# Optimization experiments

Measured on AMD Instinct MI355X. Metric: run time of the kernel, lower is better.

## Reference

```python
import jax, jax.numpy as jnp
import numpy as np

B, T, D_IN, D_ENC, D_H = 16384, 60, 3, 64, 128


def setup_inputs() -> dict:
    key = jax.random.key(0)
    ks = jax.random.split(key, 10)
    s_enc = 1.0 / np.sqrt(D_IN)
    s_lstm = 1.0 / np.sqrt(D_H)
    s_dec = 1.0 / np.sqrt(D_H)
    return {
        "x": jax.random.normal(ks[0], (B, D_IN), dtype=jnp.float32),
        "W_enc": jax.random.uniform(ks[1], (D_ENC, D_IN), jnp.float32, -s_enc, s_enc),
        "b_enc": jax.random.uniform(ks[2], (D_ENC,), jnp.float32, -s_enc, s_enc),
        "W_ih": jax.random.uniform(ks[3], (4 * D_H, D_ENC), jnp.float32, -s_lstm, s_lstm),
        "W_hh": jax.random.uniform(ks[4], (4 * D_H, D_H), jnp.float32, -s_lstm, s_lstm),
        "b_ih": jax.random.uniform(ks[5], (4 * D_H,), jnp.float32, -s_lstm, s_lstm),
        "b_hh": jax.random.uniform(ks[6], (4 * D_H,), jnp.float32, -s_lstm, s_lstm),
        "W_dec": jax.random.uniform(ks[7], (1, D_H), jnp.float32, -s_dec, s_dec),
        "b_dec": jax.random.uniform(ks[8], (1,), jnp.float32, -s_dec, s_dec),
    }


def _forward(x, W_enc, b_enc, W_ih, W_hh, b_ih, b_hh, W_dec, b_dec):
    encoded = x @ W_enc.T + b_enc  # [B, 64]
    # Input to LSTM is identical at every timestep -> precompute Wx projection once.
    xp = encoded @ W_ih.T + b_ih + b_hh  # [B, 4*H], PyTorch gate order i,f,g,o
    h0 = jnp.zeros((x.shape[0], D_H), x.dtype)
    c0 = jnp.zeros((x.shape[0], D_H), x.dtype)

    def step(carry, _):
        h, c = carry
        gates = xp + h @ W_hh.T  # [B, 4*H]
        i, f, g, o = jnp.split(gates, 4, axis=-1)
        i = jax.nn.sigmoid(i)
        f = jax.nn.sigmoid(f)
        g = jnp.tanh(g)
        o = jax.nn.sigmoid(o)
        c = f * c + i * g
        h = o * jnp.tanh(c)
        return (h, c), h

    (_, _), hs = jax.lax.scan(step, (h0, c0), None, length=T)  # hs: [T, B, H]
    lstm_out = jnp.transpose(hs, (1, 0, 2))  # [B, T, H]
    out = (lstm_out @ W_dec.T + b_dec)[..., 0]  # [B, T]
    return jax.nn.sigmoid(out)


def reference(x, W_enc, b_enc, W_ih, W_hh, b_ih, b_hh, W_dec, b_dec):
    return _forward(x, W_enc, b_enc, W_ih, W_hh, b_ih, b_hh, W_dec, b_dec)
```

## Files before the change

### kernel.cpp

```cpp
#include <hip/hip_runtime.h>

#define T_STEPS 60
#define HID 128
#define ROWS 16
#define NBLK (16384 / ROWS)

typedef __attribute__((ext_vector_type(8))) short short8;
typedef __attribute__((ext_vector_type(4))) float f32x4;

#define K1 1.44269504088896340736f

__device__ __forceinline__ unsigned short f2bf(float f) {
  unsigned u = __float_as_uint(f);
  return (unsigned short)((u + 0x7fffu + ((u >> 16) & 1u)) >> 16);
}
__device__ __forceinline__ float sigm(float x) {
  return __builtin_amdgcn_rcpf(1.0f + __expf(-x));
}
template <int CTRL>
__device__ __forceinline__ float dppadd(float x) {
  int y = __builtin_amdgcn_update_dpp(0, __builtin_bit_cast(int, x), CTRL, 0xf,
                                      0xf, false);
  return x + __builtin_bit_cast(float, y);
}

#define HB0 0
#define HB1 4096
#define XP_BASE 8192
#define PART 40960
#define WSTRIDE 968
#define LDS_BYTES (PART + 8 * WSTRIDE * 4)

__global__ __launch_bounds__(512, 4) void lstm_fused(
    const float* __restrict__ x, const float* __restrict__ W_enc,
    const float* __restrict__ b_enc, const float* __restrict__ W_ih,
    const float* __restrict__ W_hh, const float* __restrict__ b_ih,
    const float* __restrict__ b_hh, const float* __restrict__ W_dec,
    const float* __restrict__ b_dec, float* __restrict__ out) {
  __shared__ __align__(16) unsigned char lds[LDS_BYTES];

  const int tid = threadIdx.x;
  const int wav = tid >> 6;
  const int lane = tid & 63;
  const int l15 = lane & 15;
  const int l4 = lane >> 4;
  const int u = wav * 16 + l15;
  const int row0 = blockIdx.x * ROWS;

  for (int i = tid; i < 1024; i += 512) ((unsigned*)(lds + HB0))[i] = 0u;

  {
    f32x4 xp4[4];
    float xr0[4], xr1[4], xr2[4];
#pragma unroll
    for (int v = 0; v < 4; ++v) {
      int r = 4 * l4 + v;
      const float* xp_ = x + (size_t)(row0 + r) * 3;
      xr0[v] = xp_[0];
      xr1[v] = xp_[1];
      xr2[v] = xp_[2];
    }
#pragma unroll
    for (int gt = 0; gt < 4; ++gt) {
      float bias = b_ih[gt * 128 + u] + b_hh[gt * 128 + u];
#pragma unroll
      for (int v = 0; v < 4; ++v) xp4[gt][v] = bias;
    }
    const f32x4* wr0 = (const f32x4*)(W_ih + (size_t)u * 64);
    const f32x4* wr1 = (const f32x4*)(W_ih + (size_t)(128 + u) * 64);
    const f32x4* wr2 = (const f32x4*)(W_ih + (size_t)(256 + u) * 64);
    const f32x4* wr3 = (const f32x4*)(W_ih + (size_t)(384 + u) * 64);
    for (int e4 = 0; e4 < 16; ++e4) {
      f32x4 w0 = wr0[e4], w1 = wr1[e4], w2 = wr2[e4], w3 = wr3[e4];
#pragma unroll
      for (int j = 0; j < 4; ++j) {
        int e = e4 * 4 + j;
        float we0 = W_enc[e * 3], we1 = W_enc[e * 3 + 1], we2 = W_enc[e * 3 + 2];
        float be = b_enc[e];
#pragma unroll
        for (int v = 0; v < 4; ++v) {
          float ev = fmaf(we0, xr0[v], fmaf(we1, xr1[v], fmaf(we2, xr2[v], be)));
          xp4[0][v] = fmaf(w0[j], ev, xp4[0][v]);
          xp4[1][v] = fmaf(w1[j], ev, xp4[1][v]);
          xp4[2][v] = fmaf(w2[j], ev, xp4[2][v]);
          xp4[3][v] = fmaf(w3[j], ev, xp4[3][v]);
        }
      }
    }
#pragma unroll
    for (int gt = 0; gt < 4; ++gt) {
      float s = (gt == 2) ? (-2.0f * K1) : (-K1);
#pragma unroll
      for (int v = 0; v < 4; ++v) xp4[gt][v] *= s;
      *(f32x4*)(lds + XP_BASE + gt * 8192 + (unsigned)tid * 16) = xp4[gt];
    }
  }

  short8 bw[4][4];
#pragma unroll
  for (int gt = 0; gt < 4; ++gt) {
    float s = (gt == 2) ? (-2.0f * K1) : (-K1);
#pragma unroll
    for (int kt = 0; kt < 4; ++kt) {
      const float* p = W_hh + (size_t)(gt * 128 + u) * HID + kt * 32 + 8 * l4;
      short8 f;
#pragma unroll
      for (int j = 0; j < 8; ++j) f[j] = (short)f2bf(s * p[j]);
      bw[gt][kt] = f;
    }
  }

  float ct0 = 0.0f, ct1 = 0.0f, ct2 = 0.0f, ct3 = 0.0f;

  const unsigned swzA =
      (((unsigned)(l15 & 7)) << 4) ^ (((unsigned)(l15 & 8)) << 2);
  unsigned rd0 = ((unsigned)(l15 * 256 + l4 * 16)) ^ swzA;
  unsigned rd1 = ((unsigned)(l15 * 256 + l4 * 16 + 64)) ^ swzA;
  unsigned wr0, wr1, wr2, wr3;
  {
    unsigned rr = (unsigned)(4 * l4);
#define WRADDR(v) ((((rr + v) * 256 + (unsigned)u * 2) ^ (((rr + v) & 7u) << 4) ^ \
                    (((rr + v) & 8u) << 2)) + HB1)
    wr0 = WRADDR(0); wr1 = WRADDR(1); wr2 = WRADDR(2); wr3 = WRADDR(3);
#undef WRADDR
  }
  const unsigned xpA = (unsigned)tid * 16;
  const float wdu = W_dec[u];
  unsigned ptv = PART + (unsigned)(wav * WSTRIDE + 4 * l4) * 4;
  const float kneg = -2.0f * K1;
  const float kpos = 2.0f * K1;

  __syncthreads();

#pragma clang loop unroll(disable)
  for (int t = 0; t < T_STEPS; ++t) {
    f32x4 xpr0 = *(const f32x4*)(lds + XP_BASE + 0 * 8192 + xpA);
    f32x4 xpr1 = *(const f32x4*)(lds + XP_BASE + 1 * 8192 + xpA);
    f32x4 xpr2 = *(const f32x4*)(lds + XP_BASE + 2 * 8192 + xpA);
    f32x4 xpr3 = *(const f32x4*)(lds + XP_BASE + 3 * 8192 + xpA);
    short8 af0 = *(const short8*)(lds + rd0);
    short8 af1 = *(const short8*)(lds + rd1);
    short8 af2 = *(const short8*)(lds + rd0 + 128);
    short8 af3 = *(const short8*)(lds + rd1 + 128);
    f32x4 a0 = __builtin_amdgcn_mfma_f32_16x16x32_bf16(af0, bw[0][0], xpr0, 0, 0, 0);
    f32x4 a1 = __builtin_amdgcn_mfma_f32_16x16x32_bf16(af0, bw[1][0], xpr1, 0, 0, 0);
    f32x4 a2 = __builtin_amdgcn_mfma_f32_16x16x32_bf16(af0, bw[2][0], xpr2, 0, 0, 0);
    f32x4 a3 = __builtin_amdgcn_mfma_f32_16x16x32_bf16(af0, bw[3][0], xpr3, 0, 0, 0);
    a0 = __builtin_amdgcn_mfma_f32_16x16x32_bf16(af1, bw[0][1], a0, 0, 0, 0);
    a1 = __builtin_amdgcn_mfma_f32_16x16x32_bf16(af1, bw[1][1], a1, 0, 0, 0);
    a2 = __builtin_amdgcn_mfma_f32_16x16x32_bf16(af1, bw[2][1], a2, 0, 0, 0);
    a3 = __builtin_amdgcn_mfma_f32_16x16x32_bf16(af1, bw[3][1], a3, 0, 0, 0);
    a0 = __builtin_amdgcn_mfma_f32_16x16x32_bf16(af2, bw[0][2], a0, 0, 0, 0);
    a1 = __builtin_amdgcn_mfma_f32_16x16x32_bf16(af2, bw[1][2], a1, 0, 0, 0);
    a2 = __builtin_amdgcn_mfma_f32_16x16x32_bf16(af2, bw[2][2], a2, 0, 0, 0);
    a3 = __builtin_amdgcn_mfma_f32_16x16x32_bf16(af2, bw[3][2], a3, 0, 0, 0);
    a0 = __builtin_amdgcn_mfma_f32_16x16x32_bf16(af3, bw[0][3], a0, 0, 0, 0);
    a1 = __builtin_amdgcn_mfma_f32_16x16x32_bf16(af3, bw[1][3], a1, 0, 0, 0);
    a2 = __builtin_amdgcn_mfma_f32_16x16x32_bf16(af3, bw[2][3], a2, 0, 0, 0);
    a3 = __builtin_amdgcn_mfma_f32_16x16x32_bf16(af3, bw[3][3], a3, 0, 0, 0);

    float h[4];
    f32x4 pz;
#pragma unroll
    for (int v = 0; v < 4; ++v) {
      float ea = __builtin_amdgcn_exp2f(a0[v]);
      float ef = __builtin_amdgcn_exp2f(a1[v]);
      float eg = __builtin_amdgcn_exp2f(a2[v]);
      float eo = __builtin_amdgcn_exp2f(a3[v]);
      float A = 1.0f + ea, F = 1.0f + ef, G = 1.0f + eg, Bo = 1.0f + eo;
      float AG = A * G;
      float r = __builtin_amdgcn_rcpf(F * AG);
      float tt = fmaf(kpos, eg, kneg);
      float cprev = (v == 0) ? ct0 : (v == 1) ? ct1 : (v == 2) ? ct2 : ct3;
      float num = fmaf(cprev, AG, tt * F);
      float cn = num * r;
      if (v == 0) ct0 = cn; else if (v == 1) ct1 = cn; else if (v == 2) ct2 = cn; else ct3 = cn;
      float ec = __builtin_amdgcn_exp2f(cn);
      float r2 = __builtin_amdgcn_rcpf(Bo * (1.0f + ec));
      h[v] = (1.0f - ec) * r2;
      pz[v] = h[v] * wdu;
    }
    unsigned r01, r23;
    asm("v_cvt_pk_bf16_f32 %0, %1, %2" : "=v"(r01) : "v"(h[0]), "v"(h[1]));
    asm("v_cvt_pk_bf16_f32 %0, %1, %2" : "=v"(r23) : "v"(h[2]), "v"(h[3]));
    *(unsigned short*)(lds + wr0) = (unsigned short)r01;
    *(unsigned short*)(lds + wr1) = (unsigned short)(r01 >> 16);
    *(unsigned short*)(lds + wr2) = (unsigned short)r23;
    *(unsigned short*)(lds + wr3) = (unsigned short)(r23 >> 16);
#pragma unroll
    for (int v = 0; v < 4; ++v)
      pz[v] = dppadd<0x140>(dppadd<0x141>(dppadd<0x4E>(dppadd<0xB1>(pz[v]))));
    if (l15 == 0) *(f32x4*)(lds + ptv) = pz;
    __syncthreads();
    rd0 ^= 4096; rd1 ^= 4096;
    wr0 ^= 4096; wr1 ^= 4096; wr2 ^= 4096; wr3 ^= 4096;
    ptv += 64;
  }

  const float bdec = b_dec[0];
  const float* partf = (const float*)(lds + PART);
  for (int i = tid; i < 16 * T_STEPS; i += 512) {
    int r = i / T_STEPS, t = i - r * T_STEPS;
    float s = 0.0f;
#pragma unroll
    for (int w = 0; w < 8; ++w) s += partf[w * WSTRIDE + t * 16 + r];
    out[(size_t)(row0 + r) * T_STEPS + t] = sigm(s + bdec);
  }
}

extern "C" void kernel_launch(void* const* d_in, const int* in_sizes, int n_in,
                              void* d_out, int out_size, void* d_ws, size_t ws_size,
                              hipStream_t stream) {
  const float* x = (const float*)d_in[0];
  const float* W_enc = (const float*)d_in[1];
  const float* b_enc = (const float*)d_in[2];
  const float* W_ih = (const float*)d_in[3];
  const float* W_hh = (const float*)d_in[4];
  const float* b_ih = (const float*)d_in[5];
  const float* b_hh = (const float*)d_in[6];
  const float* W_dec = (const float*)d_in[7];
  const float* b_dec = (const float*)d_in[8];
  float* out = (float*)d_out;

  dim3 grid(NBLK);
  dim3 block(512);
  lstm_fused<<<grid, block, 0, stream>>>(x, W_enc, b_enc, W_ih, W_hh, b_ih, b_hh,
                                         W_dec, b_dec, out);
}
```

Before: 242.7 us.

## Halve block size so each wave computes two hidden-unit tiles per step

Each workgroup now uses 4 waves of 256 threads instead of 8 waves of 512, and each wave handles 32 hidden units through two sets of MFMA tiles. The decoder partial sums are folded into the per-row output in a rotating wave during the recurrence using a double-buffered partial area, which shrinks LDS from a per-timestep buffer to a small output staging area. The goal is to cut barrier cost and raise instruction-level parallelism per wave across the two independent MFMA chains. In exchange each wave holds twice the weight fragments in registers and launch bounds drop to 2 blocks, which may reduce occupancy or cause register pressure.

```diff
diff --git a/kernel.cpp b/kernel.cpp
--- a/kernel.cpp
+++ b/kernel.cpp
@@ -24,14 +24,13 @@
   return x + __builtin_bit_cast(float, y);
 }
 
-#define HB0 0
-#define HB1 4096
-#define XP_BASE 8192
-#define PART 40960
-#define WSTRIDE 968
-#define LDS_BYTES (PART + 8 * WSTRIDE * 4)
-
-__global__ __launch_bounds__(512, 4) void lstm_fused(
+#define HB 0
+#define XP 8192
+#define PT 40960
+#define OS 41472
+#define LDS_BYTES 45312
+
+__global__ __launch_bounds__(256, 2) void lstm_fused(
     const float* __restrict__ x, const float* __restrict__ W_enc,
     const float* __restrict__ b_enc, const float* __restrict__ W_ih,
     const float* __restrict__ W_hh, const float* __restrict__ b_ih,
@@ -44,46 +43,51 @@
   const int lane = tid & 63;
   const int l15 = lane & 15;
   const int l4 = lane >> 4;
-  const int u = wav * 16 + l15;
+  const int u0 = wav * 32 + l15;
+  const int u1 = u0 + 16;
   const int row0 = blockIdx.x * ROWS;
-
-  for (int i = tid; i < 1024; i += 512) ((unsigned*)(lds + HB0))[i] = 0u;
-
-  {
+  float* OSf = (float*)(lds + OS);
+
+  for (int i = tid; i < 1024; i += 256) ((unsigned*)(lds + HB))[i] = 0u;
+
+  float xr0[4], xr1[4], xr2[4];
+#pragma unroll
+  for (int v = 0; v < 4; ++v) {
+    int r = 4 * l4 + v;
+    const float* xp_ = x + (size_t)(row0 + r) * 3;
+    xr0[v] = xp_[0];
+    xr1[v] = xp_[1];
+    xr2[v] = xp_[2];
+  }
+
+#pragma unroll
+  for (int j = 0; j < 2; ++j) {
+    const int u = u0 + j * 16;
     f32x4 xp4[4];
-    float xr0[4], xr1[4], xr2[4];
-#pragma unroll
-    for (int v = 0; v < 4; ++v) {
-      int r = 4 * l4 + v;
-      const float* xp_ = x + (size_t)(row0 + r) * 3;
-      xr0[v] = xp_[0];
-      xr1[v] = xp_[1];
-      xr2[v] = xp_[2];
-    }
 #pragma unroll
     for (int gt = 0; gt < 4; ++gt) {
       float bias = b_ih[gt * 128 + u] + b_hh[gt * 128 + u];
 #pragma unroll
       for (int v = 0; v < 4; ++v) xp4[gt][v] = bias;
     }
-    const f32x4* wr0 = (const f32x4*)(W_ih + (size_t)u * 64);
-    const f32x4* wr1 = (const f32x4*)(W_ih + (size_t)(128 + u) * 64);
-    const f32x4* wr2 = (const f32x4*)(W_ih + (size_t)(256 + u) * 64);
-    const f32x4* wr3 = (const f32x4*)(W_ih + (size_t)(384 + u) * 64);
+    const f32x4* wp0 = (const f32x4*)(W_ih + (size_t)u * 64);
+    const f32x4* wp1 = (const f32x4*)(W_ih + (size_t)(128 + u) * 64);
+    const f32x4* wp2 = (const f32x4*)(W_ih + (size_t)(256 + u) * 64);
+    const f32x4* wp3 = (const f32x4*)(W_ih + (size_t)(384 + u) * 64);
     for (int e4 = 0; e4 < 16; ++e4) {
-      f32x4 w0 = wr0[e4], w1 = wr1[e4], w2 = wr2[e4], w3 = wr3[e4];
-#pragma unroll
-      for (int j = 0; j < 4; ++j) {
-        int e = e4 * 4 + j;
+      f32x4 w0 = wp0[e4], w1 = wp1[e4], w2 = wp2[e4], w3 = wp3[e4];
+#pragma unroll
+      for (int jj = 0; jj < 4; ++jj) {
+        int e = e4 * 4 + jj;
         float we0 = W_enc[e * 3], we1 = W_enc[e * 3 + 1], we2 = W_enc[e * 3 + 2];
         float be = b_enc[e];
 #pragma unroll
         for (int v = 0; v < 4; ++v) {
           float ev = fmaf(we0, xr0[v], fmaf(we1, xr1[v], fmaf(we2, xr2[v], be)));
-          xp4[0][v] = fmaf(w0[j], ev, xp4[0][v]);
-          xp4[1][v] = fmaf(w1[j], ev, xp4[1][v]);
-          xp4[2][v] = fmaf(w2[j], ev, xp4[2][v]);
-          xp4[3][v] = fmaf(w3[j], ev, xp4[3][v]);
+          xp4[0][v] = fmaf(w0[jj], ev, xp4[0][v]);
+          xp4[1][v] = fmaf(w1[jj], ev, xp4[1][v]);
+          xp4[2][v] = fmaf(w2[jj], ev, xp4[2][v]);
+          xp4[3][v] = fmaf(w3[jj], ev, xp4[3][v]);
         }
       }
     }
@@ -92,41 +96,53 @@
       float s = (gt == 2) ? (-2.0f * K1) : (-K1);
 #pragma unroll
       for (int v = 0; v < 4; ++v) xp4[gt][v] *= s;
-      *(f32x4*)(lds + XP_BASE + gt * 8192 + (unsigned)tid * 16) = xp4[gt];
-    }
-  }
-
-  short8 bw[4][4];
+      *(f32x4*)(lds + XP + (unsigned)(gt * 2 + j) * 4096 + (unsigned)tid * 16) =
+          xp4[gt];
+    }
+  }
+
+  short8 bwA[4][4], bwB[4][4];
 #pragma unroll
   for (int gt = 0; gt < 4; ++gt) {
     float s = (gt == 2) ? (-2.0f * K1) : (-K1);
 #pragma unroll
     for (int kt = 0; kt < 4; ++kt) {
-      const float* p = W_hh + (size_t)(gt * 128 + u) * HID + kt * 32 + 8 * l4;
-      short8 f;
-#pragma unroll
-      for (int j = 0; j < 8; ++j) f[j] = (short)f2bf(s * p[j]);
-      bw[gt][kt] = f;
-    }
-  }
-
-  float ct0 = 0.0f, ct1 = 0.0f, ct2 = 0.0f, ct3 = 0.0f;
+      const float* pA = W_hh + (size_t)(gt * 128 + u0) * HID + kt * 32 + 8 * l4;
+      const float* pB = W_hh + (size_t)(gt * 128 + u1) * HID + kt * 32 + 8 * l4;
+      short8 fA, fB;
+#pragma unroll
+      for (int jj = 0; jj < 8; ++jj) {
+        fA[jj] = (short)f2bf(s * pA[jj]);
+        fB[jj] = (short)f2bf(s * pB[jj]);
+      }
+      bwA[gt][kt] = fA;
+      bwB[gt][kt] = fB;
+    }
+  }
+
+  float ct[8] = {0.f, 0.f, 0.f, 0.f, 0.f, 0.f, 0.f, 0.f};
 
   const unsigned swzA =
       (((unsigned)(l15 & 7)) << 4) ^ (((unsigned)(l15 & 8)) << 2);
   unsigned rd0 = ((unsigned)(l15 * 256 + l4 * 16)) ^ swzA;
   unsigned rd1 = ((unsigned)(l15 * 256 + l4 * 16 + 64)) ^ swzA;
-  unsigned wr0, wr1, wr2, wr3;
+  unsigned wrA[4], wrB[4];
   {
     unsigned rr = (unsigned)(4 * l4);
-#define WRADDR(v) ((((rr + v) * 256 + (unsigned)u * 2) ^ (((rr + v) & 7u) << 4) ^ \
-                    (((rr + v) & 8u) << 2)) + HB1)
-    wr0 = WRADDR(0); wr1 = WRADDR(1); wr2 = WRADDR(2); wr3 = WRADDR(3);
+#define WRADDR(v, uu)                                                          \
+  ((((rr + v) * 256 + (unsigned)(uu)*2) ^ (((rr + v) & 7u) << 4) ^             \
+    (((rr + v) & 8u) << 2)) +                                                  \
+   4096)
+#pragma unroll
+    for (int v = 0; v < 4; ++v) {
+      wrA[v] = WRADDR(v, u0);
+      wrB[v] = WRADDR(v, u1);
+    }
 #undef WRADDR
   }
-  const unsigned xpA = (unsigned)tid * 16;
-  const float wdu = W_dec[u];
-  unsigned ptv = PART + (unsigned)(wav * WSTRIDE + 4 * l4) * 4;
+  const float wd0 = W_dec[u0];
+  const float wd1 = W_dec[u1];
+  const unsigned ptA = PT + (unsigned)(wav * 64 + l4 * 16);
   const float kneg = -2.0f * K1;
   const float kpos = 2.0f * K1;
 
@@ -134,78 +150,104 @@
 
 #pragma clang loop unroll(disable)
   for (int t = 0; t < T_STEPS; ++t) {
-    f32x4 xpr0 = *(const f32x4*)(lds + XP_BASE + 0 * 8192 + xpA);
-    f32x4 xpr1 = *(const f32x4*)(lds + XP_BASE + 1 * 8192 + xpA);
-    f32x4 xpr2 = *(const f32x4*)(lds + XP_BASE + 2 * 8192 + xpA);
-    f32x4 xpr3 = *(const f32x4*)(lds + XP_BASE + 3 * 8192 + xpA);
+    if (t > 0) {
+      int tp = t - 1;
+      if (wav == (tp & 3) && lane < 16) {
+        unsigned base = PT + ((unsigned)(tp & 1) << 8) + (unsigned)(lane * 4);
+        float s = 0.0f;
+#pragma unroll
+        for (int w2 = 0; w2 < 4; ++w2) s += *(const float*)(lds + base + w2 * 64);
+        OSf[lane * T_STEPS + tp] = s;
+      }
+    }
     short8 af0 = *(const short8*)(lds + rd0);
     short8 af1 = *(const short8*)(lds + rd1);
     short8 af2 = *(const short8*)(lds + rd0 + 128);
     short8 af3 = *(const short8*)(lds + rd1 + 128);
-    f32x4 a0 = __builtin_amdgcn_mfma_f32_16x16x32_bf16(af0, bw[0][0], xpr0, 0, 0, 0);
-    f32x4 a1 = __builtin_amdgcn_mfma_f32_16x16x32_bf16(af0, bw[1][0], xpr1, 0, 0, 0);
-    f32x4 a2 = __builtin_amdgcn_mfma_f32_16x16x32_bf16(af0, bw[2][0], xpr2, 0, 0, 0);
-    f32x4 a3 = __builtin_amdgcn_mfma_f32_16x16x32_bf16(af0, bw[3][0], xpr3, 0, 0, 0);
-    a0 = __builtin_amdgcn_mfma_f32_16x16x32_bf16(af1, bw[0][1], a0, 0, 0, 0);
-    a1 = __builtin_amdgcn_mfma_f32_16x16x32_bf16(af1, bw[1][1], a1, 0, 0, 0);
-    a2 = __builtin_amdgcn_mfma_f32_16x16x32_bf16(af1, bw[2][1], a2, 0, 0, 0);
-    a3 = __builtin_amdgcn_mfma_f32_16x16x32_bf16(af1, bw[3][1], a3, 0, 0, 0);
-    a0 = __builtin_amdgcn_mfma_f32_16x16x32_bf16(af2, bw[0][2], a0, 0, 0, 0);
-    a1 = __builtin_amdgcn_mfma_f32_16x16x32_bf16(af2, bw[1][2], a1, 0, 0, 0);
-    a2 = __builtin_amdgcn_mfma_f32_16x16x32_bf16(af2, bw[2][2], a2, 0, 0, 0);
-    a3 = __builtin_amdgcn_mfma_f32_16x16x32_bf16(af2, bw[3][2], a3, 0, 0, 0);
-    a0 = __builtin_amdgcn_mfma_f32_16x16x32_bf16(af3, bw[0][3], a0, 0, 0, 0);
-    a1 = __builtin_amdgcn_mfma_f32_16x16x32_bf16(af3, bw[1][3], a1, 0, 0, 0);
-    a2 = __builtin_amdgcn_mfma_f32_16x16x32_bf16(af3, bw[2][3], a2, 0, 0, 0);
-    a3 = __builtin_amdgcn_mfma_f32_16x16x32_bf16(af3, bw[3][3], a3, 0, 0, 0);
-
-    float h[4];
+    f32x4 aA[4], aB[4];
+#pragma unroll
+    for (int gt = 0; gt < 4; ++gt) {
+      f32x4 xA = *(const f32x4*)(lds + XP + (unsigned)(gt * 2 + 0) * 4096 +
+                                 (unsigned)tid * 16);
+      aA[gt] = __builtin_amdgcn_mfma_f32_16x16x32_bf16(af0, bwA[gt][0], xA, 0, 0, 0);
+      f32x4 xB = *(const f32x4*)(lds + XP + (unsigned)(gt * 2 + 1) * 4096 +
+                                 (unsigned)tid * 16);
+      aB[gt] = __builtin_amdgcn_mfma_f32_16x16x32_bf16(af0, bwB[gt][0], xB, 0, 0, 0);
+    }
+#pragma unroll
+    for (int gt = 0; gt < 4; ++gt) {
+      aA[gt] = __builtin_amdgcn_mfma_f32_16x16x32_bf16(af1, bwA[gt][1], aA[gt], 0, 0, 0);
+      aB[gt] = __builtin_amdgcn_mfma_f32_16x16x32_bf16(af1, bwB[gt][1], aB[gt], 0, 0, 0);
+      aA[gt] = __builtin_amdgcn_mfma_f32_16x16x32_bf16(af2, bwA[gt][2], aA[gt], 0, 0, 0);
+      aB[gt] = __builtin_amdgcn_mfma_f32_16x16x32_bf16(af2, bwB[gt][2], aB[gt], 0, 0, 0);
+      aA[gt] = __builtin_amdgcn_mfma_f32_16x16x32_bf16(af3, bwA[gt][3], aA[gt], 0, 0, 0);
+      aB[gt] = __builtin_amdgcn_mfma_f32_16x16x32_bf16(af3, bwB[gt][3], aB[gt], 0, 0, 0);
+    }
+
+    float hA[4], hB[4];
     f32x4 pz;
 #pragma unroll
-    for (int v = 0; v < 4; ++v) {
-      float ea = __builtin_amdgcn_exp2f(a0[v]);
-      float ef = __builtin_amdgcn_exp2f(a1[v]);
-      float eg = __builtin_amdgcn_exp2f(a2[v]);
-      float eo = __builtin_amdgcn_exp2f(a3[v]);
-      float A = 1.0f + ea, F = 1.0f + ef, G = 1.0f + eg, Bo = 1.0f + eo;
-      float AG = A * G;
-      float r = __builtin_amdgcn_rcpf(F * AG);
-      float tt = fmaf(kpos, eg, kneg);
-      float cprev = (v == 0) ? ct0 : (v == 1) ? ct1 : (v == 2) ? ct2 : ct3;
-      float num = fmaf(cprev, AG, tt * F);
-      float cn = num * r;
-      if (v == 0) ct0 = cn; else if (v == 1) ct1 = cn; else if (v == 2) ct2 = cn; else ct3 = cn;
-      float ec = __builtin_amdgcn_exp2f(cn);
-      float r2 = __builtin_amdgcn_rcpf(Bo * (1.0f + ec));
-      h[v] = (1.0f - ec) * r2;
-      pz[v] = h[v] * wdu;
-    }
-    unsigned r01, r23;
-    asm("v_cvt_pk_bf16_f32 %0, %1, %2" : "=v"(r01) : "v"(h[0]), "v"(h[1]));
-    asm("v_cvt_pk_bf16_f32 %0, %1, %2" : "=v"(r23) : "v"(h[2]), "v"(h[3]));
-    *(unsigned short*)(lds + wr0) = (unsigned short)r01;
-    *(unsigned short*)(lds + wr1) = (unsigned short)(r01 >> 16);
-    *(unsigned short*)(lds + wr2) = (unsigned short)r23;
-    *(unsigned short*)(lds + wr3) = (unsigned short)(r23 >> 16);
+    for (int j = 0; j < 2; ++j) {
+#pragma unroll
+      for (int v = 0; v < 4; ++v) {
+        float pa0 = j ? aB[0][v] : aA[0][v];
+        float pa1 = j ? aB[1][v] : aA[1][v];
+        float pa2 = j ? aB[2][v] : aA[2][v];
+        float pa3 = j ? aB[3][v] : aA[3][v];
+        float ea = __builtin_amdgcn_exp2f(pa0);
+        float ef = __builtin_amdgcn_exp2f(pa1);
+        float eg = __builtin_amdgcn_exp2f(pa2);
+        float eo = __builtin_amdgcn_exp2f(pa3);
+        float A = 1.0f + ea, F = 1.0f + ef, G = 1.0f + eg, Bo = 1.0f + eo;
+        float AG = A * G;
+        float r = __builtin_amdgcn_rcpf(F * AG);
+        float tt = fmaf(kpos, eg, kneg);
+        float num = fmaf(ct[j * 4 + v], AG, tt * F);
+        float cn = num * r;
+        ct[j * 4 + v] = cn;
+        float ec = __builtin_amdgcn_exp2f(cn);
+        float r2 = __builtin_amdgcn_rcpf(Bo * (1.0f + ec));
+        float hh = (1.0f - ec) * r2;
+        if (j) hB[v] = hh; else hA[v] = hh;
+      }
+    }
+#pragma unroll
+    for (int v = 0; v < 4; ++v) pz[v] = fmaf(hA[v], wd0, hB[v] * wd1);
+    unsigned rA01, rA23, rB01, rB23;
+    asm("v_cvt_pk_bf16_f32 %0, %1, %2" : "=v"(rA01) : "v"(hA[0]), "v"(hA[1]));
+    asm("v_cvt_pk_bf16_f32 %0, %1, %2" : "=v"(rA23) : "v"(hA[2]), "v"(hA[3]));
+    asm("v_cvt_pk_bf16_f32 %0, %1, %2" : "=v"(rB01) : "v"(hB[0]), "v"(hB[1]));
+    asm("v_cvt_pk_bf16_f32 %0, %1, %2" : "=v"(rB23) : "v"(hB[2]), "v"(hB[3]));
+    *(unsigned short*)(lds + wrA[0]) = (unsigned short)rA01;
+    *(unsigned short*)(lds + wrA[1]) = (unsigned short)(rA01 >> 16);
+    *(unsigned short*)(lds + wrA[2]) = (unsigned short)rA23;
+    *(unsigned short*)(lds + wrA[3]) = (unsigned short)(rA23 >> 16);
+    *(unsigned short*)(lds + wrB[0]) = (unsigned short)rB01;
+    *(unsigned short*)(lds + wrB[1]) = (unsigned short)(rB01 >> 16);
+    *(unsigned short*)(lds + wrB[2]) = (unsigned short)rB23;
+    *(unsigned short*)(lds + wrB[3]) = (unsigned short)(rB23 >> 16);
 #pragma unroll
     for (int v = 0; v < 4; ++v)
       pz[v] = dppadd<0x140>(dppadd<0x141>(dppadd<0x4E>(dppadd<0xB1>(pz[v]))));
-    if (l15 == 0) *(f32x4*)(lds + ptv) = pz;
+    if (l15 == 0) *(f32x4*)(lds + ptA + ((unsigned)(t & 1) << 8)) = pz;
     __syncthreads();
     rd0 ^= 4096; rd1 ^= 4096;
-    wr0 ^= 4096; wr1 ^= 4096; wr2 ^= 4096; wr3 ^= 4096;
-    ptv += 64;
-  }
+#pragma unroll
+    for (int v = 0; v < 4; ++v) { wrA[v] ^= 4096; wrB[v] ^= 4096; }
+  }
+
+  if (wav == (59 & 3) && lane < 16) {
+    unsigned base = PT + ((unsigned)(59 & 1) << 8) + (unsigned)(lane * 4);
+    float s = 0.0f;
+#pragma unroll
+    for (int w2 = 0; w2 < 4; ++w2) s += *(const float*)(lds + base + w2 * 64);
+    OSf[lane * T_STEPS + 59] = s;
+  }
+  __syncthreads();
 
   const float bdec = b_dec[0];
-  const float* partf = (const float*)(lds + PART);
-  for (int i = tid; i < 16 * T_STEPS; i += 512) {
-    int r = i / T_STEPS, t = i - r * T_STEPS;
-    float s = 0.0f;
-#pragma unroll
-    for (int w = 0; w < 8; ++w) s += partf[w * WSTRIDE + t * 16 + r];
-    out[(size_t)(row0 + r) * T_STEPS + t] = sigm(s + bdec);
-  }
+  for (int i = tid; i < ROWS * T_STEPS; i += 256)
+    out[(size_t)row0 * T_STEPS + i] = sigm(OSf[i] + bdec);
 }
 
 extern "C" void kernel_launch(void* const* d_in, const int* in_sizes, int n_in,
@@ -223,7 +265,7 @@
   float* out = (float*)d_out;
 
   dim3 grid(NBLK);
-  dim3 block(512);
+  dim3 block(256);
   lstm_fused<<<grid, block, 0, stream>>>(x, W_enc, b_enc, W_ih, W_hh, b_ih, b_hh,
                                          W_dec, b_dec, out);
 }
```

After: 248.3 us. +2.3%, slower.
